# Optimization experiments

Measured on AMD Instinct MI355X. Metric: run time of the kernel, lower is better.

The kernel has to match this reference:

```python
import jax, jax.numpy as jnp
import numpy as np

N_HEAD = 4
N_FEAT = 256
D_K = N_FEAT // N_HEAD
SCALE = 1.0  # self.scale (non-trainable, scale>0 and tr_scale=None)
INV_SQRT_DK = 1.0 / (D_K ** 0.5)


def sparsemax(z, scale=1.0):
    """Closed-form equivalent of the module's sort-based sparsemax loop.
    Projects onto the simplex of radius `scale`, then divides by scale.
    Matches the strict `>` support condition of the while-loop."""
    n = z.shape[-1]
    z_sorted = jnp.flip(jnp.sort(z, axis=-1), axis=-1)          # descending
    csum = jnp.cumsum(z_sorted, axis=-1)
    k = jnp.arange(1, n + 1, dtype=z.dtype)
    support = k * z_sorted > (csum - scale)                      # strict, as in torch loop
    k_max = jnp.sum(support, axis=-1, keepdims=True)             # int, >=1 in practice
    csum_k = jnp.take_along_axis(csum, k_max - 1, axis=-1)
    tau = (csum_k - scale) / k_max.astype(z.dtype)               # tau_z
    return jax.nn.relu(z - tau) / scale


def setup_inputs() -> dict:
    key = jax.random.key(0)
    ks = jax.random.split(key, 9)
    B, T1, T2 = 4, 2048, 2048
    query = jax.random.normal(ks[0], (B, T1, N_FEAT), jnp.float32)
    key_t = jax.random.normal(ks[1], (B, T2, N_FEAT), jnp.float32)
    value = jax.random.normal(ks[2], (B, T2, N_FEAT), jnp.float32)
    mask = jnp.ones((B, 1, T2), jnp.int32)
    s = 0.02
    Wq = jax.random.normal(ks[3], (N_FEAT, N_FEAT), jnp.float32) * s
    bq = jax.random.normal(ks[4], (N_FEAT,), jnp.float32) * s
    Wk = jax.random.normal(ks[5], (N_FEAT, N_FEAT), jnp.float32) * s
    bk = jax.random.normal(ks[6], (N_FEAT,), jnp.float32) * s
    Wv = jax.random.normal(ks[7], (N_FEAT, N_FEAT), jnp.float32) * s
    bv = jax.random.normal(ks[8], (N_FEAT,), jnp.float32) * s
    return {"query": query, "key": key_t, "value": value, "mask": mask,
            "Wq": Wq, "bq": bq, "Wk": Wk, "bk": bk, "Wv": Wv, "bv": bv}


def reference(query, key, value, mask, Wq, bq, Wk, bk, Wv, bv):
    B, T1, _ = query.shape
    # forward_qkv: project, split heads, L2-normalize q/k (cosine attention) * scale
    q = (query @ Wq.T + bq).reshape(B, T1, N_HEAD, D_K).transpose(0, 2, 1, 3)  # (B,H,T1,dk)
    k = (key @ Wk.T + bk).reshape(B, -1, N_HEAD, D_K).transpose(0, 2, 1, 3)    # (B,H,T2,dk)
    v = (value @ Wv.T + bv).reshape(B, -1, N_HEAD, D_K).transpose(0, 2, 1, 3)  # (B,H,T2,dk)
    q = q / jnp.linalg.norm(q, axis=-1, keepdims=True) * SCALE
    k = k / jnp.linalg.norm(k, axis=-1, keepdims=True) * SCALE
    scores = jnp.einsum('bhqd,bhkd->bhqk', q, k) * INV_SQRT_DK  # (B,H,T1,T2)
    # forward_attention with mask: fill masked with float min, sparsemax, zero masked
    m = (mask[:, None, :, :] == 0)                               # (B,1,1|T1,T2)
    min_val = jnp.finfo(scores.dtype).min
    scores = jnp.where(m, min_val, scores)
    attn = jnp.where(m, 0.0, sparsemax(scores, 1.0))
    x = jnp.einsum('bhqk,bhkd->bhqd', attn, v)
    x = x.transpose(0, 2, 1, 3).reshape(B, T1, N_HEAD * D_K)     # NOTE: linear_out is never applied in the original forward
    return attn, x
```

## Files before the change

kernel.cpp:

```cpp
#include <hip/hip_runtime.h>
#include <hip/hip_bf16.h>

#define NB 4
#define NH 4
#define TT 2048
#define DKK 64
#define NF 256
#define QT 16

typedef __attribute__((ext_vector_type(8))) short bf16x8;
typedef __attribute__((ext_vector_type(4))) short s16x4;
typedef __attribute__((ext_vector_type(4))) float f32x4;
typedef __hip_bfloat16 bf16;

__device__ __forceinline__ short f2bs(float f) {
    bf16 h = __float2bfloat16(f);
    return *reinterpret_cast<short*>(&h);
}
__device__ __forceinline__ float b2f(short s) {
    return __uint_as_float(((unsigned)(unsigned short)s) << 16);
}
__device__ __forceinline__ float wave_sum(float v) {
    #pragma unroll
    for (int off = 1; off < 64; off <<= 1) v += __shfl_xor(v, off);
    return v;
}

__global__ __launch_bounds__(256)
void wcvt_kernel(const float* __restrict__ Wq, const float* __restrict__ Wk,
                 const float* __restrict__ Wv, bf16* __restrict__ Wb)
{
    int gid = (blockIdx.x * 256 + threadIdx.x) * 4;
    const float* src;
    int m = gid >> 16, off = gid & 65535;
    src = (m == 0) ? Wq : (m == 1) ? Wk : Wv;
    float4 v = *(const float4*)(src + off);
    s16x4 o = { f2bs(v.x), f2bs(v.y), f2bs(v.z), f2bs(v.w) };
    *(s16x4*)((short*)Wb + gid) = o;
}

__global__ __launch_bounds__(256, 4)
void qkv_kernel(const float* __restrict__ query, const float* __restrict__ key,
                const float* __restrict__ value, const bf16* __restrict__ Wb,
                const float* __restrict__ bq, const float* __restrict__ bk,
                const float* __restrict__ bv,
                bf16* __restrict__ qB, bf16* __restrict__ kA, bf16* __restrict__ vB)
{
    __shared__ char Xq[8192], Xk[8192], Xv[8192];
    __shared__ char bounce[24576];
    const int tid = threadIdx.x;
    const int bt0 = blockIdx.x * 16;
    const int b0 = bt0 >> 11, t0 = bt0 & (TT - 1);

    {
        int row = tid >> 4, c0 = (tid & 15) * 16;
        int swr = (row & 7) << 4;
        const float* qs = query + (size_t)(bt0 + row) * NF + c0;
        const float* ks = key   + (size_t)(bt0 + row) * NF + c0;
        const float* vs = value + (size_t)(bt0 + row) * NF + c0;
        #pragma unroll
        for (int j = 0; j < 4; ++j) {
            float4 a = *(const float4*)(qs + j * 4);
            float4 b = *(const float4*)(ks + j * 4);
            float4 c = *(const float4*)(vs + j * 4);
            int byt = (row * 512 + c0 * 2 + j * 8) ^ swr;
            *(s16x4*)(Xq + byt) = (s16x4){ f2bs(a.x), f2bs(a.y), f2bs(a.z), f2bs(a.w) };
            *(s16x4*)(Xk + byt) = (s16x4){ f2bs(b.x), f2bs(b.y), f2bs(b.z), f2bs(b.w) };
            *(s16x4*)(Xv + byt) = (s16x4){ f2bs(c.x), f2bs(c.y), f2bs(c.z), f2bs(c.w) };
        }
    }
    __syncthreads();

    const int lane = tid & 63;
    const int w = tid >> 6;
    const int l15 = lane & 15;
    const int g = lane >> 4;
    const int swl = (l15 & 7) << 4;

    f32x4 qa[4], ka[4], va[4];
    #pragma unroll
    for (int ct = 0; ct < 4; ++ct) {
        qa[ct] = (f32x4){0.f,0.f,0.f,0.f};
        ka[ct] = (f32x4){0.f,0.f,0.f,0.f};
        va[ct] = (f32x4){0.f,0.f,0.f,0.f};
    }
    const bf16* Wqb = Wb;
    const bf16* Wkb = Wb + 65536;
    const bf16* Wvb = Wb + 131072;

    #pragma unroll
    for (int kt = 0; kt < 8; ++kt) {
        int byt = (l15 * 512 + kt * 64 + g * 16) ^ swl;
        bf16x8 xq = *(const bf16x8*)(Xq + byt);
        bf16x8 xk = *(const bf16x8*)(Xk + byt);
        bf16x8 xv = *(const bf16x8*)(Xv + byt);
        #pragma unroll
        for (int ct = 0; ct < 4; ++ct) {
            size_t wo = (size_t)(w * 64 + ct * 16 + l15) * NF + kt * 32 + g * 8;
            bf16x8 aq = *(const bf16x8*)(Wqb + wo);
            bf16x8 ak = *(const bf16x8*)(Wkb + wo);
            bf16x8 av = *(const bf16x8*)(Wvb + wo);
            qa[ct] = __builtin_amdgcn_mfma_f32_16x16x32_bf16(aq, xq, qa[ct], 0, 0, 0);
            ka[ct] = __builtin_amdgcn_mfma_f32_16x16x32_bf16(ak, xk, ka[ct], 0, 0, 0);
            va[ct] = __builtin_amdgcn_mfma_f32_16x16x32_bf16(av, xv, va[ct], 0, 0, 0);
        }
    }

    float qv[4][4], kv[4][4], vv[4][4];
    float sq = 0.f, sk = 0.f;
    #pragma unroll
    for (int ct = 0; ct < 4; ++ct) {
        float4 b4q = *(const float4*)(bq + w * 64 + ct * 16 + g * 4);
        float4 b4k = *(const float4*)(bk + w * 64 + ct * 16 + g * 4);
        float4 b4v = *(const float4*)(bv + w * 64 + ct * 16 + g * 4);
        #pragma unroll
        for (int p = 0; p < 4; ++p) {
            float bqp = (p == 0) ? b4q.x : (p == 1) ? b4q.y : (p == 2) ? b4q.z : b4q.w;
            float bkp = (p == 0) ? b4k.x : (p == 1) ? b4k.y : (p == 2) ? b4k.z : b4k.w;
            float bvp = (p == 0) ? b4v.x : (p == 1) ? b4v.y : (p == 2) ? b4v.z : b4v.w;
            qv[ct][p] = qa[ct][p] + bqp;
            kv[ct][p] = ka[ct][p] + bkp;
            vv[ct][p] = va[ct][p] + bvp;
            sq = __builtin_fmaf(qv[ct][p], qv[ct][p], sq);
            sk = __builtin_fmaf(kv[ct][p], kv[ct][p], sk);
        }
    }
    sq += __shfl_xor(sq, 16); sq += __shfl_xor(sq, 32);
    sk += __shfl_xor(sk, 16); sk += __shfl_xor(sk, 32);
    float nq = rsqrtf(sq) * 0.125f;
    float nk = rsqrtf(sk);

    __syncthreads();
    #pragma unroll
    for (int ct = 0; ct < 4; ++ct) {
        #pragma unroll
        for (int p = 0; p < 4; ++p) {
            int d5 = (ct & 1) * 16 + g * 4 + p;
            int qb = w * 2048 + (ct >> 1) * 1024 + (d5 >> 3) * 256 + l15 * 16 + (d5 & 7) * 2;
            *(short*)(bounce + qb)        = f2bs(qv[ct][p] * nq);
            *(short*)(bounce + qb + 8192) = f2bs(kv[ct][p] * nk);
            int vb = 16384 + w * 2048 + ct * 512 + (l15 >> 3) * 256 + (g * 4 + p) * 16 + (l15 & 7) * 2;
            *(short*)(bounce + vb)        = f2bs(vv[ct][p]);
        }
    }
    __syncthreads();

    const int qt = t0 >> 4;
    const int kc = t0 >> 5, h16 = (t0 >> 4) & 1;
    for (int seg = tid; seg < 1536; seg += 256) {
        int byt = seg * 16;
        const char* src = bounce + byt;
        bf16* dst;
        if (byt < 8192) {
            int wh = byt >> 11, off = byt & 2047;
            dst = qB + (((size_t)(b0 * NH + wh)) * 128 + qt) * 1024 + off / 2;
        } else if (byt < 16384) {
            int r = byt - 8192;
            int wh = r >> 11, off = r & 2047;
            dst = kA + (((size_t)(b0 * NH + wh)) * 128 + qt) * 1024 + off / 2;
        } else {
            int r = byt - 16384;
            int wh = r >> 11, ct = (r >> 9) & 3, off = r & 511;
            dst = vB + ((((size_t)(b0 * NH + wh)) * 64 + kc) * 4 + ct) * 512 + h16 * 256 + off / 2;
        }
        *(bf16x8*)dst = *(const bf16x8*)src;
    }
}

__global__ __launch_bounds__(512, 4)
void attn_kernel(const bf16* __restrict__ qB, const bf16* __restrict__ kA,
                 const bf16* __restrict__ vB, const int* __restrict__ mask,
                 float* __restrict__ attn, float* __restrict__ xout)
{
    __shared__ short S_s[16 * 2048];
    __shared__ float4 xpart[4][64];
    const int tid = threadIdx.x;
    const int lane = tid & 63;
    const int w = tid >> 6;
    const int l15 = lane & 15;
    const int g = lane >> 4;
    const int bh = blockIdx.x >> 7;
    const int qt = blockIdx.x & 127;
    const int q0 = qt * QT;
    const int b_ = bh >> 2, h_ = bh & 3;

    const size_t fb = (size_t)bh * 16384;
    const bf16x8* qBv = (const bf16x8*)qB + fb + (size_t)qt * 128;
    const bf16x8* kAv = (const bf16x8*)kA + fb;
    const bf16x8* vBv = (const bf16x8*)vB + fb;
    const int* mrow = mask + b_ * TT + w * 256;

    bf16x8 qf0 = qBv[lane];
    bf16x8 qf1 = qBv[64 + lane];

    f32x4 acc[16];
    #pragma unroll
    for (int t = 0; t < 16; ++t) acc[t] = (f32x4){0.f, 0.f, 0.f, 0.f};

    #pragma unroll
    for (int t = 0; t < 16; ++t) {
        int kt = w * 16 + t;
        bf16x8 kf0 = kAv[(kt * 2 + 0) * 64 + lane];
        bf16x8 kf1 = kAv[(kt * 2 + 1) * 64 + lane];
        acc[t] = __builtin_amdgcn_mfma_f32_16x16x32_bf16(kf0, qf0, acc[t], 0, 0, 0);
        acc[t] = __builtin_amdgcn_mfma_f32_16x16x32_bf16(kf1, qf1, acc[t], 0, 0, 0);
    }

    char* prow = (char*)S_s + l15 * 4096;
    const int sw = (l15 & 7) << 4;
    #pragma unroll
    for (int t = 0; t < 16; ++t) {
        int4 mv = *(const int4*)(mrow + t * 16 + g * 4);
        s16x4 sb;
        sb[0] = mv.x ? f2bs(acc[t][0]) : f2bs(-3.0e38f);
        sb[1] = mv.y ? f2bs(acc[t][1]) : f2bs(-3.0e38f);
        sb[2] = mv.z ? f2bs(acc[t][2]) : f2bs(-3.0e38f);
        sb[3] = mv.w ? f2bs(acc[t][3]) : f2bs(-3.0e38f);
        *(s16x4*)(prow + ((w * 512 + t * 32 + g * 8) ^ sw)) = sb;
    }
    __syncthreads();

    const int r0 = 2 * w;
    float va[2][32];
    #pragma unroll
    for (int h = 0; h < 2; ++h) {
        const char* sr = (const char*)S_s + (r0 + h) * 4096;
        int swr = ((r0 + h) & 7) << 4;
        #pragma unroll
        for (int jj = 0; jj < 8; ++jj) {
            s16x4 p4 = *(const s16x4*)(sr + ((jj * 512 + lane * 8) ^ swr));
            va[h][jj * 4 + 0] = b2f(p4[0]);
            va[h][jj * 4 + 1] = b2f(p4[1]);
            va[h][jj * 4 + 2] = b2f(p4[2]);
            va[h][jj * 4 + 3] = b2f(p4[3]);
        }
    }

    float tau[2];
    #pragma unroll
    for (int h = 0; h < 2; ++h) {
        float S = 0.f, C = 0.f, Qs = 0.f;
        #pragma unroll
        for (int i = 0; i < 32; ++i) {
            float v = va[h][i];
            bool un = v > -1.0e30f;
            float sv = un ? v : 0.f;
            S += sv;
            C += un ? 1.f : 0.f;
            Qs = __builtin_fmaf(sv, sv, Qs);
        }
        S = wave_sum(S); C = wave_sum(C); Qs = wave_sum(Qs);
        float tu, prevC;
        bool done;
        if (C < 0.5f) { tu = 3.0e38f; done = true; prevC = 0.f; }
        else {
            float mu = S / C;
            float var = Qs / C - mu * mu;
            var = var > 0.f ? var : 0.f;
            tu = mu + 1.7f * __builtin_sqrtf(var);
            prevC = -1.f;
            done = false;
        }
        for (int it = 0; it < 64 && !done; ++it) {
            float S2 = 0.f, C2 = 0.f;
            #pragma unroll
            for (int i = 0; i < 32; ++i) {
                float v = va[h][i];
                bool in = v > tu;
                S2 += in ? v : 0.f;
                C2 += in ? 1.f : 0.f;
            }
            S2 = wave_sum(S2); C2 = wave_sum(C2);
            if (C2 == prevC) done = true;
            else if (C2 < 0.5f) { tu = (S - 1.f) / C; prevC = -1.f; }
            else { tu = (S2 - 1.f) / C2; prevC = C2; }
        }
        tau[h] = tu;
    }

    #pragma unroll
    for (int h = 0; h < 2; ++h) {
        char* sr = (char*)S_s + (r0 + h) * 4096;
        int swr = ((r0 + h) & 7) << 4;
        float* ar = attn + ((size_t)bh * TT + q0 + r0 + h) * TT;
        float tu = tau[h];
        #pragma unroll
        for (int jj = 0; jj < 8; ++jj) {
            f32x4 o;
            s16x4 pb4;
            #pragma unroll
            for (int e = 0; e < 4; ++e) {
                float a = va[h][jj * 4 + e] - tu;
                a = a > 0.f ? a : 0.f;
                o[e] = a;
                pb4[e] = f2bs(a);
            }
            *(f32x4*)(ar + jj * 256 + lane * 4) = o;
            *(s16x4*)(sr + ((jj * 512 + lane * 8) ^ swr)) = pb4;
        }
    }
    __syncthreads();

    const int ds = w & 3;
    const int kh = w >> 2;
    f32x4 xacc = (f32x4){0.f, 0.f, 0.f, 0.f};
    #pragma unroll 8
    for (int kcl = 0; kcl < 32; ++kcl) {
        int kc = kh * 32 + kcl;
        bf16x8 af = *(const bf16x8*)(prow + ((kh * 2048 + kcl * 64 + g * 16) ^ sw));
        bf16x8 bfr = vBv[(kc * 4 + ds) * 64 + lane];
        xacc = __builtin_amdgcn_mfma_f32_16x16x32_bf16(af, bfr, xacc, 0, 0, 0);
    }
    if (w >= 4) xpart[w - 4][lane] = make_float4(xacc[0], xacc[1], xacc[2], xacc[3]);
    __syncthreads();
    if (w < 4) {
        float4 xp4 = xpart[w][lane];
        xacc[0] += xp4.x; xacc[1] += xp4.y; xacc[2] += xp4.z; xacc[3] += xp4.w;
        float* xp = xout + ((size_t)b_ * TT + q0 + g * 4) * NF + h_ * DKK + ds * 16 + l15;
        #pragma unroll
        for (int p = 0; p < 4; ++p) xp[p * NF] = xacc[p];
    }
}

extern "C" void kernel_launch(void* const* d_in, const int* in_sizes, int n_in,
                              void* d_out, int out_size, void* d_ws, size_t ws_size,
                              hipStream_t stream) {
    const float* query = (const float*)d_in[0];
    const float* key   = (const float*)d_in[1];
    const float* value = (const float*)d_in[2];
    const int*   mask  = (const int*)d_in[3];
    const float* Wq = (const float*)d_in[4];
    const float* bq = (const float*)d_in[5];
    const float* Wk = (const float*)d_in[6];
    const float* bk = (const float*)d_in[7];
    const float* Wv = (const float*)d_in[8];
    const float* bv = (const float*)d_in[9];

    float* attn = (float*)d_out;
    float* x    = (float*)d_out + (size_t)NB * NH * TT * TT;

    const size_t FRAG = (size_t)NB * NH * 16384 * 8;
    bf16* Wb = (bf16*)d_ws;
    bf16* qB = Wb + 3 * 65536;
    bf16* kA = qB + FRAG;
    bf16* vB = kA + FRAG;

    wcvt_kernel<<<dim3(192), dim3(256), 0, stream>>>(Wq, Wk, Wv, Wb);
    qkv_kernel<<<dim3(NB * TT / 16), dim3(256), 0, stream>>>(
        query, key, value, Wb, bq, bk, bv, qB, kA, vB);
    attn_kernel<<<dim3(NB * NH * (TT / QT)), dim3(512), 0, stream>>>(
        qB, kA, vB, mask, attn, x);
}
```

Before: 142.7 us.

## Pack mask into bitmask, swizzle block order, use nontemporal output stores

An extra block in the weight-conversion kernel packs the int32 mask into 32-bit bitmasks, so the attention kernel loads 8 words per wave instead of int4 mask vectors for every tile. The attention grid index is swizzled to interleave blocks across (batch, head) groups, changing how K/V reuse maps onto caches and XCDs. The large attn and x output writes become nontemporal stores so they do not pollute the cache. The mask path adds a small amount of preprocessing work, and the swizzle may either help or hurt locality.

```diff
diff --git a/kernel.cpp b/kernel.cpp
--- a/kernel.cpp
+++ b/kernel.cpp
@@ -28,8 +28,18 @@
 
 __global__ __launch_bounds__(256)
 void wcvt_kernel(const float* __restrict__ Wq, const float* __restrict__ Wk,
-                 const float* __restrict__ Wv, bf16* __restrict__ Wb)
+                 const float* __restrict__ Wv, const int* __restrict__ mask,
+                 bf16* __restrict__ Wb, unsigned* __restrict__ mbits)
 {
+    if (blockIdx.x == 192) {
+        int t = threadIdx.x;
+        const int* mp = mask + t * 32;
+        unsigned m = 0;
+        #pragma unroll
+        for (int j = 0; j < 32; ++j) m |= (mp[j] != 0 ? 1u : 0u) << j;
+        mbits[t] = m;
+        return;
+    }
     int gid = (blockIdx.x * 256 + threadIdx.x) * 4;
     const float* src;
     int m = gid >> 16, off = gid & 65535;
@@ -169,7 +179,7 @@
 
 __global__ __launch_bounds__(512, 4)
 void attn_kernel(const bf16* __restrict__ qB, const bf16* __restrict__ kA,
-                 const bf16* __restrict__ vB, const int* __restrict__ mask,
+                 const bf16* __restrict__ vB, const unsigned* __restrict__ mbits,
                  float* __restrict__ attn, float* __restrict__ xout)
 {
     __shared__ short S_s[16 * 2048];
@@ -179,8 +189,9 @@
     const int w = tid >> 6;
     const int l15 = lane & 15;
     const int g = lane >> 4;
-    const int bh = blockIdx.x >> 7;
-    const int qt = blockIdx.x & 127;
+    const int swz = (blockIdx.x & 7) * 256 + (blockIdx.x >> 3);
+    const int bh = swz >> 7;
+    const int qt = swz & 127;
     const int q0 = qt * QT;
     const int b_ = bh >> 2, h_ = bh & 3;
 
@@ -188,7 +199,13 @@
     const bf16x8* qBv = (const bf16x8*)qB + fb + (size_t)qt * 128;
     const bf16x8* kAv = (const bf16x8*)kA + fb;
     const bf16x8* vBv = (const bf16x8*)vB + fb;
-    const int* mrow = mask + b_ * TT + w * 256;
+
+    unsigned mreg[8];
+    {
+        const unsigned* mwp = mbits + b_ * 64 + w * 8;
+        #pragma unroll
+        for (int i = 0; i < 8; ++i) mreg[i] = mwp[i];
+    }
 
     bf16x8 qf0 = qBv[lane];
     bf16x8 qf1 = qBv[64 + lane];
@@ -206,16 +223,17 @@
         acc[t] = __builtin_amdgcn_mfma_f32_16x16x32_bf16(kf1, qf1, acc[t], 0, 0, 0);
     }
 
+    const short NEGB = (short)0xFF7F;
     char* prow = (char*)S_s + l15 * 4096;
     const int sw = (l15 & 7) << 4;
     #pragma unroll
     for (int t = 0; t < 16; ++t) {
-        int4 mv = *(const int4*)(mrow + t * 16 + g * 4);
+        unsigned bits = mreg[t >> 1] >> (((t & 1) << 4) + (g << 2));
         s16x4 sb;
-        sb[0] = mv.x ? f2bs(acc[t][0]) : f2bs(-3.0e38f);
-        sb[1] = mv.y ? f2bs(acc[t][1]) : f2bs(-3.0e38f);
-        sb[2] = mv.z ? f2bs(acc[t][2]) : f2bs(-3.0e38f);
-        sb[3] = mv.w ? f2bs(acc[t][3]) : f2bs(-3.0e38f);
+        sb[0] = (bits & 1) ? f2bs(acc[t][0]) : NEGB;
+        sb[1] = (bits & 2) ? f2bs(acc[t][1]) : NEGB;
+        sb[2] = (bits & 4) ? f2bs(acc[t][2]) : NEGB;
+        sb[3] = (bits & 8) ? f2bs(acc[t][3]) : NEGB;
         *(s16x4*)(prow + ((w * 512 + t * 32 + g * 8) ^ sw)) = sb;
     }
     __syncthreads();
@@ -295,7 +313,7 @@
                 o[e] = a;
                 pb4[e] = f2bs(a);
             }
-            *(f32x4*)(ar + jj * 256 + lane * 4) = o;
+            __builtin_nontemporal_store(o, (f32x4*)(ar + jj * 256 + lane * 4));
             *(s16x4*)(sr + ((jj * 512 + lane * 8) ^ swr)) = pb4;
         }
     }
@@ -318,7 +336,8 @@
         xacc[0] += xp4.x; xacc[1] += xp4.y; xacc[2] += xp4.z; xacc[3] += xp4.w;
         float* xp = xout + ((size_t)b_ * TT + q0 + g * 4) * NF + h_ * DKK + ds * 16 + l15;
         #pragma unroll
-        for (int p = 0; p < 4; ++p) xp[p * NF] = xacc[p];
+        for (int p = 0; p < 4; ++p)
+            __builtin_nontemporal_store(xacc[p], xp + p * NF);
     }
 }
 
@@ -344,10 +363,11 @@
     bf16* qB = Wb + 3 * 65536;
     bf16* kA = qB + FRAG;
     bf16* vB = kA + FRAG;
-
-    wcvt_kernel<<<dim3(192), dim3(256), 0, stream>>>(Wq, Wk, Wv, Wb);
+    unsigned* mbits = (unsigned*)(vB + FRAG);
+
+    wcvt_kernel<<<dim3(193), dim3(256), 0, stream>>>(Wq, Wk, Wv, mask, Wb, mbits);
     qkv_kernel<<<dim3(NB * TT / 16), dim3(256), 0, stream>>>(
         query, key, value, Wb, bq, bk, bv, qB, kA, vB);
     attn_kernel<<<dim3(NB * NH * (TT / QT)), dim3(512), 0, stream>>>(
-        qB, kA, vB, mask, attn, x);
-}
+        qB, kA, vB, mbits, attn, x);
+}
```

Result: faster. 134.9 us (-5.4%).
